# Kernel tuning notes

Hardware: AMD Instinct MI355X
Metric: run time of the kernel (lower is better)

The kernel has to match this reference:

```python
import jax, jax.numpy as jnp
import numpy as np

D = H = W = 64
N = D * H * W
BS = 2
C = 32          # enc_dim
IN_DIM = 4
OUT_DIM = 4
P = 5           # pos_enc_dim
COND = 32
M = 8           # modes per axis
NL = 4          # n_layers
NODE_IN = IN_DIM + 3 + 2 * P * 3   # 37
ENC_T = 1 + 2 * P                  # 11
ENC_C = ENC_T * COND               # 352
DT = 0.05


def fourier_embedding(pos, n_freq):
    # F(x) = [cos(2^i*pi*x_l), sin(2^i*pi*x_l)] per coordinate l, then concat x
    freq = (2.0 ** jnp.arange(n_freq, dtype=jnp.float32)) * jnp.pi  # (P,)
    ang = pos[..., None] * freq                                     # (..., L, P)
    emb = jnp.concatenate([jnp.cos(ang), jnp.sin(ang)], axis=-1)    # (..., L, 2P)
    emb = emb.reshape(*pos.shape[:-1], -1)                          # (..., L*2P)
    return jnp.concatenate([emb, pos], axis=-1)


def setup_inputs() -> dict:
    key = jax.random.key(0)
    ks = jax.random.split(key, 24)
    scale = 1.0 / C ** 2
    inp = {
        "state_in": jax.random.normal(ks[0], (BS, N, IN_DIM), jnp.float32),
        "node_pos": jax.random.uniform(ks[1], (BS, N, 3), jnp.float32),
        "edges": jax.random.randint(ks[2], (BS, 16, 2), 0, N),
        "time_i": jax.random.uniform(ks[3], (BS, 1), jnp.float32),
        "conditions": jax.random.uniform(ks[4], (BS, COND), jnp.float32),
        "t_embed_w": jax.random.normal(ks[5], (C, ENC_T), jnp.float32) * 0.05,
        "t_embed_b": jax.random.normal(ks[6], (C,), jnp.float32) * 0.05,
        "c_embed_w": jax.random.normal(ks[7], (C, ENC_C), jnp.float32) * 0.05,
        "c_embed_b": jax.random.normal(ks[8], (C,), jnp.float32) * 0.05,
        "lift_w": jax.random.normal(ks[9], (C, NODE_IN), jnp.float32) * 0.05,
        "lift_b": jax.random.normal(ks[10], (C,), jnp.float32) * 0.05,
        "spec_wr": jax.random.uniform(ks[11], (NL, C, C, M, M, M), jnp.float32) * scale,
        "spec_wi": jax.random.uniform(ks[12], (NL, C, C, M, M, M), jnp.float32) * scale,
        "byp_w": jax.random.normal(ks[13], (NL, C, C), jnp.float32) * 0.05,
        "byp_b": jax.random.normal(ks[14], (NL, C), jnp.float32) * 0.05,
        "proj1_w": jax.random.normal(ks[15], (C, C), jnp.float32) * 0.05,
        "proj1_b": jax.random.normal(ks[16], (C,), jnp.float32) * 0.05,
        "proj2_w": jax.random.normal(ks[17], (OUT_DIM, C), jnp.float32) * 0.05,
        "proj2_b": jax.random.normal(ks[18], (OUT_DIM,), jnp.float32) * 0.05,
    }
    return inp


def _conv1x1(x, w, b):
    # x: (b, c, d, h, w), w: (o, c), b: (o,)
    return jnp.einsum('bcdhw,oc->bodhw', x, w) + b[None, :, None, None, None]


def _fno_forward(state_in, node_pos, time_i, conditions,
                 t_embed_w, t_embed_b, c_embed_w, c_embed_b, lift_w, lift_b,
                 spec_wr, spec_wi, byp_w, byp_b, proj1_w, proj1_b, proj2_w, proj2_b):
    pos_enc = fourier_embedding(node_pos, P)      # (bs, N, 33)
    c_enc = fourier_embedding(conditions, P)      # (bs, 352)
    t_enc = fourier_embedding(time_i, P)          # (bs, 11)

    node_feat = jnp.concatenate([state_in, pos_enc], axis=-1)  # (bs, N, 37)
    t_emb = (t_enc @ t_embed_w.T + t_embed_b)[:, :, None, None, None]
    c_emb = (c_enc @ c_embed_w.T + c_embed_b)[:, :, None, None, None]

    # (bs, N, 37) -> (bs, 37, D, H, W)
    x = node_feat.transpose(0, 2, 1).reshape(BS, NODE_IN, D, H, W)
    x = _conv1x1(x, lift_w, lift_b)
    x = x + t_emb + c_emb

    for l in range(NL):
        w = jax.lax.complex(spec_wr[l], spec_wi[l])              # (C, C, M, M, M)
        x_ft = jnp.fft.rfftn(x, axes=(-3, -2, -1))               # (bs, C, D, H, W//2+1)
        blk = jnp.einsum('bixyz,ioxyz->boxyz', x_ft[..., :M, :M, :M], w)
        out_ft = jnp.zeros_like(x_ft).at[..., :M, :M, :M].set(blk)
        sp = jnp.fft.irfftn(out_ft, s=(D, H, W), axes=(-3, -2, -1))
        bp = _conv1x1(x, byp_w[l], byp_b[l])
        x = jax.nn.gelu(sp + bp, approximate=False)

    x = jax.nn.gelu(_conv1x1(x, proj1_w, proj1_b), approximate=False)
    x = _conv1x1(x, proj2_w, proj2_b)                            # (bs, 4, D, H, W)
    v_pred = x.reshape(BS, OUT_DIM, N).transpose(0, 2, 1)        # (bs, N, 4)
    return state_in + DT * v_pred


def reference(state_in, node_pos, edges, time_i, conditions,
              t_embed_w, t_embed_b, c_embed_w, c_embed_b, lift_w, lift_b,
              spec_wr, spec_wi, byp_w, byp_b, proj1_w, proj1_b, proj2_w, proj2_b):
    # edges are unused in the FNO forward (kept for API compatibility)
    return _fno_forward(state_in, node_pos, time_i, conditions,
                        t_embed_w, t_embed_b, c_embed_w, c_embed_b, lift_w, lift_b,
                        spec_wr, spec_wi, byp_w, byp_b, proj1_w, proj1_b, proj2_w, proj2_b)
```

## Files before the change

kernel.cpp:

```cpp
#include <hip/hip_runtime.h>
#include <math.h>

#define PI_F 3.14159265358979323846f

typedef __bf16 bf16x8 __attribute__((ext_vector_type(8)));
typedef float floatx4 __attribute__((ext_vector_type(4)));
union U8 { unsigned short u[8]; uint4 q; bf16x8 v; };

__device__ __forceinline__ float gelu_sig(float v) {
    float e = __builtin_amdgcn_exp2f(-2.4554670f * v);
    return v * __builtin_amdgcn_rcpf(1.0f + e);
}
__device__ __forceinline__ int rfl(int x) { return __builtin_amdgcn_readfirstlane(x); }

__device__ __forceinline__ unsigned short f2bf(float f) {
    unsigned int u = __float_as_uint(f);
    u += 0x7fffu + ((u >> 16) & 1u);
    return (unsigned short)(u >> 16);
}
__device__ __forceinline__ float bf2f(unsigned short h) {
    return __uint_as_float(((unsigned int)h) << 16);
}
__device__ __forceinline__ unsigned int pack2(float a, float b) {
    return (unsigned int)f2bf(a) | ((unsigned int)f2bf(b) << 16);
}

__global__ void k_wt(const float* __restrict__ time_i, const float* __restrict__ conditions,
                     const float* __restrict__ t_embed_w, const float* __restrict__ t_embed_b,
                     const float* __restrict__ c_embed_w, const float* __restrict__ c_embed_b,
                     const float* __restrict__ lift_b, float* __restrict__ embk,
                     const float* __restrict__ byp_w, const float* __restrict__ lift_w,
                     unsigned short* __restrict__ wbh, unsigned short* __restrict__ wlbf,
                     unsigned short* __restrict__ Tinv, unsigned short* __restrict__ TfT,
                     float* __restrict__ Tp1g) {
    const float th = PI_F / 32.0f;
    int t = threadIdx.x;
    if (blockIdx.x < 2) {
        __shared__ float red[8][32];
        int b = blockIdx.x;
        int c = t & 31, lg = t >> 5;
        float acc = 0.0f;
        if (lg == 0) {
            acc = t_embed_b[c] + c_embed_b[c] + lift_b[c];
            float tv = time_i[b];
            float ang = PI_F * tv;
            const float* tw = t_embed_w + c * 11;
            for (int i = 0; i < 5; i++) {
                float s, co; sincosf(ang, &s, &co);
                acc += co * tw[i] + s * tw[5 + i];
                ang *= 2.0f;
            }
            acc += tv * tw[10];
        }
        const float* cw = c_embed_w + c * 352;
        for (int j = 0; j < 4; j++) {
            int l = lg * 4 + j;
            float v = conditions[b * 32 + l];
            float ang = PI_F * v;
            for (int i = 0; i < 5; i++) {
                float s, co; sincosf(ang, &s, &co);
                acc += co * cw[l * 10 + i] + s * cw[l * 10 + 5 + i];
                ang *= 2.0f;
            }
            acc += v * cw[320 + l];
        }
        red[lg][c] = acc;
        __syncthreads();
        if (t < 32) {
            float s = 0.0f;
            for (int g = 0; g < 8; g++) s += red[g][t];
            embk[b * 32 + t] = s;
        }
        return;
    }
    int idx = (blockIdx.x - 2) * 256 + t;
    if (idx < 4096) {
        wbh[idx] = f2bf(byp_w[idx]);
    } else if (idx < 6144) {
        int j = idx - 4096;
        int o = j >> 6, q = j & 63;
        wlbf[j] = (q < 37) ? f2bf(lift_w[o * 37 + q]) : 0;
    } else if (idx < 8192) {
        int j = idx - 6144;
        int nz = j >> 5, k = j & 31;
        int kz = k >> 1;
        float val = 0.0f;
        if (kz < 8) {
            float a = (float)((kz * nz) & 63) * th;
            val = (k & 1) ? sinf(a) : cosf(a);
            val *= (kz == 0) ? (1.0f / 262144.0f) : (2.0f / 262144.0f);
        }
        Tinv[j] = f2bf(val);
    } else if (idx < 9216) {
        int j = idx - 8192;
        int kcol = j >> 6, nz = j & 63;
        int kz = kcol >> 1;
        float a = (float)((kz * nz) & 63) * th;
        float val = (kcol & 1) ? -sinf(a) : cosf(a);
        TfT[j] = f2bf(val);
    } else if (idx < 9728) {
        int j = idx - 9216;
        int ny = j >> 3, ky = j & 7;
        float a = (float)((ky * ny) & 63) * th;
        Tp1g[j * 2] = cosf(a);
        Tp1g[j * 2 + 1] = sinf(a);
    }
}

__device__ __forceinline__ void swz8k(int blk, int& b, int& nx, int& ny) {
    int x = blk & 7;
    int j = blk >> 3;
    int pair = x * 16 + (j >> 6);
    ny = j & 63;
    b = pair >> 6;
    nx = pair & 63;
}

__global__ __launch_bounds__(256) void k_lift(const float* __restrict__ state_in,
        const float* __restrict__ node_pos, const unsigned short* __restrict__ wlbf,
        const float* __restrict__ embk, const unsigned short* __restrict__ TfT,
        unsigned short* __restrict__ x0, unsigned int* __restrict__ a1) {
    __shared__ __align__(16) float SL[5024];
    unsigned short* fsT  = (unsigned short*)SL;
    unsigned short* ysbf = (unsigned short*)(SL + 2304);
    float* pz   = SL + 3456;
    float* pz2  = SL + 4480;
    float* bias = SL + 4992;
    int t = threadIdx.x;
    int b, nx, ny; swz8k(blockIdx.x, b, nx, ny);
    int nxy = nx * 64 + ny;

    if (t < 32) bias[t] = embk[b * 32 + t];
    {
        for (int u = t; u < 2048; u += 256) {
            int row = u >> 5, col = 37 + (u & 31);
            fsT[row * 72 + col] = 0;
        }
    }
    if (t < 192) {
        int nzf = t / 3;
        int l = t - nzf * 3;
        float p = node_pos[((size_t)b * 262144 + (nxy << 6)) * 3 + t];
        float s, c; sincosf(PI_F * p, &s, &c);
        unsigned short* row = fsT + nzf * 72;
        #pragma unroll
        for (int i = 0; i < 5; i++) {
            row[4 + l * 10 + i] = f2bf(c);
            row[4 + l * 10 + 5 + i] = f2bf(s);
            float nc = 2.0f * c * c - 1.0f;
            s = 2.0f * s * c;
            c = nc;
        }
        row[34 + l] = f2bf(p);
    } else {
        int nzf = t - 192;
        const float4 s4 = *(const float4*)(state_in + ((size_t)b * 262144 + (nxy << 6) + nzf) * 4);
        unsigned short* row = fsT + nzf * 72;
        row[0] = f2bf(s4.x); row[1] = f2bf(s4.y);
        row[2] = f2bf(s4.z); row[3] = f2bf(s4.w);
    }
    __syncthreads();

    int lane = t & 63;
    int w = rfl(t >> 6);
    int otile = w & 1;
    int nzt0 = (w >> 1) * 2;
    int l15 = lane & 15;
    int quad = lane >> 4;

    U8 a0, a1_;
    a0.q = *(const uint4*)(wlbf + ((otile * 16 + l15) << 6) + (quad << 3));
    a1_.q = *(const uint4*)(wlbf + ((otile * 16 + l15) << 6) + 32 + (quad << 3));
    floatx4 cb;
    #pragma unroll
    for (int r = 0; r < 4; r++) cb[r] = bias[otile * 16 + quad * 4 + r];
    floatx4 dz = {0.0f, 0.0f, 0.0f, 0.0f};

    #pragma unroll
    for (int m = 0; m < 2; m++) {
        int nzc = (nzt0 + m) * 16 + l15;
        U8 b0, b1_;
        b0.q = *(const uint4*)(fsT + nzc * 72 + (quad << 3));
        b1_.q = *(const uint4*)(fsT + nzc * 72 + 32 + (quad << 3));
        floatx4 d = __builtin_amdgcn_mfma_f32_16x16x32_bf16(a0.v, b0.v, cb, 0, 0, 0);
        d = __builtin_amdgcn_mfma_f32_16x16x32_bf16(a1_.v, b1_.v, d, 0, 0, 0);
        #pragma unroll
        for (int r = 0; r < 4; r++) {
            int o = otile * 16 + quad * 4 + r;
            ysbf[o * 72 + nzc] = f2bf(d[r]);
        }
    }
    __syncthreads();
    {
        int ch = t >> 3, q = t & 7;
        uint4 v = *(const uint4*)(ysbf + ch * 72 + q * 8);
        *(uint4*)(x0 + (((size_t)(b * 32 + ch)) << 18) + (nxy << 6) + q * 8) = v;
    }
    {
        int khalf = w >> 1;
        U8 ay, bt;
        ay.q = *(const uint4*)(ysbf + (otile * 16 + l15) * 72 + khalf * 32 + (quad << 3));
        bt.q = *(const uint4*)(TfT + (l15 << 6) + khalf * 32 + (quad << 3));
        floatx4 d = __builtin_amdgcn_mfma_f32_16x16x32_bf16(ay.v, bt.v, dz, 0, 0, 0);
        *(floatx4*)(pz + w * 256 + lane * 4) = d;
    }
    __syncthreads();
    if (w < 2) {
        float4 p0 = *(float4*)(pz + w * 256 + lane * 4);
        float4 p1 = *(float4*)(pz + (w + 2) * 256 + lane * 4);
        float pv[4] = {p0.x + p1.x, p0.y + p1.y, p0.z + p1.z, p0.w + p1.w};
        #pragma unroll
        for (int r = 0; r < 4; r++)
            pz2[(otile * 16 + quad * 4 + r) * 16 + l15] = pv[r];
    }
    __syncthreads();
    if (t < 128) {
        float4 v = *(float4*)(pz2 + t * 4);
        unsigned int* a1p = a1 + ((size_t)(b * 4096 + nxy)) * 256;
        *(uint2*)(a1p + t * 2) = make_uint2(pack2(v.x, v.y), pack2(v.z, v.w));
    }
}


__global__ __launch_bounds__(256) void k_p1(const unsigned int* __restrict__ a1,
        const float2* __restrict__ Tp1g, float2* __restrict__ a2p) {
    int blk = blockIdx.x, t = threadIdx.x;
    int x = blk & 7, r = blk >> 3;
    int pair = x * 16 + (r & 15);
    int qtr = r >> 4;
    const unsigned int* src = a1 + ((size_t)(pair * 64 + qtr * 16)) * 256 + t;
    float accr[8], acci[8];
    #pragma unroll
    for (int k = 0; k < 8; k++) { accr[k] = 0.0f; acci[k] = 0.0f; }
    #pragma unroll 4
    for (int j = 0; j < 16; j++) {
        int ny = qtr * 16 + j;
        unsigned int pv = src[(size_t)j * 256];
        float vx = bf2f((unsigned short)(pv & 0xffffu));
        float vy = bf2f((unsigned short)(pv >> 16));
        const float2* tw = Tp1g + ny * 8;
        #pragma unroll
        for (int ky = 0; ky < 8; ky++) {
            float2 w2 = tw[ky];
            accr[ky] += vx * w2.x + vy * w2.y;
            acci[ky] += vy * w2.x - vx * w2.y;
        }
    }
    float4* dst = (float4*)(a2p + (size_t)qtr * 262144 + ((size_t)(pair * 256 + t)) * 8);
    #pragma unroll
    for (int j = 0; j < 4; j++)
        dst[j] = make_float4(accr[2 * j], acci[2 * j], accr[2 * j + 1], acci[2 * j + 1]);
}

__global__ __launch_bounds__(256) void k_p2(const float2* __restrict__ a2p,
                                            float2* __restrict__ xft) {
    __shared__ __align__(16) float2 SH[1040];
    int blk = blockIdx.x, t = threadIdx.x;
    for (int lu = 0; lu < 2; lu++) {
        int un = blk * 2 + lu;
        int b = un >> 8, ckz = un & 255;
        size_t base = (size_t)b * 131072 + (size_t)ckz * 8;
        for (int e = t; e < 512; e += 256) {
            size_t a = base + (size_t)(e >> 3) * 2048 + (e & 7);
            float2 v0 = a2p[a];
            float2 v1 = a2p[a + 262144];
            float2 v2 = a2p[a + 524288];
            float2 v3 = a2p[a + 786432];
            SH[lu * 520 + e] = make_float2(v0.x + v1.x + v2.x + v3.x,
                                           v0.y + v1.y + v2.y + v3.y);
        }
    }
    __syncthreads();
    if (t < 128) {
        int lu = t >> 6, out = t & 63;
        int un = blk * 2 + lu;
        int kx = out & 7;
        float sn, cc; sincosf((float)kx * (PI_F / 32.0f), &sn, &cc);
        float bsn = -sn;
        float tc = 1.0f, ts = 0.0f, rr = 0.0f, ri = 0.0f;
        const float2* row = SH + lu * 520 + (out >> 3);
        for (int nx = 0; nx < 64; nx++) {
            float2 v = row[nx * 8];
            rr += v.x * tc - v.y * ts;
            ri += v.x * ts + v.y * tc;
            float nt = tc * cc - ts * bsn; ts = ts * cc + tc * bsn; tc = nt;
        }
        xft[(size_t)un * 64 + out] = make_float2(rr, ri);
    }
}

__global__ __launch_bounds__(256) void k_p3(const float2* __restrict__ xft,
        const float* __restrict__ wr, const float* __restrict__ wi,
        float2* __restrict__ yftp) {
    __shared__ __align__(16) float2 SH[64];
    int blk = blockIdx.x, t = threadIdx.x;
    int unit = blk >> 2, iq = blk & 3;
    int b = unit >> 6, kx = (unit >> 3) & 7, ky = unit & 7;
    if (t < 64) {
        int il = t >> 3, kz = t & 7;
        int i = iq * 8 + il;
        SH[t] = xft[((size_t)((b * 32 + i) * 8 + kz)) * 64 + ky * 8 + kx];
    }
    __syncthreads();
    int o = t >> 3, kz = t & 7;
    float yr = 0.0f, yi = 0.0f;
    for (int il = 0; il < 8; il++) {
        int i = iq * 8 + il;
        float2 xv = SH[il * 8 + kz];
        int wofs = ((i * 32 + o) << 9) + kx * 64 + ky * 8 + kz;
        float wrv = wr[wofs], wiv = wi[wofs];
        yr += xv.x * wrv - xv.y * wiv;
        yi += xv.x * wiv + xv.y * wrv;
    }
    yftp[(size_t)iq * 32768 + ((size_t)((b * 32 + o) * 8 + kz)) * 64 + ky * 8 + kx]
        = make_float2(yr, yi);
}

__global__ __launch_bounds__(256) void k_p4(const float2* __restrict__ yftp,
                                            float2* __restrict__ b1) {
    __shared__ __align__(16) float2 SH[4608];
    int blk = blockIdx.x, t = threadIdx.x;
    for (int u = 0; u < 2; u++) {
        if (u) __syncthreads();
        int unit = blk * 2 + u;
        int b = unit >> 8, nx = (unit >> 2) & 63, og = unit & 3;
        size_t sbase = ((size_t)(b * 32 + og * 8)) * 512;
        for (int e = t; e < 4096; e += 256) {
            float2 v0 = yftp[sbase + e];
            float2 v1 = yftp[32768 + sbase + e];
            float2 v2 = yftp[65536 + sbase + e];
            float2 v3 = yftp[98304 + sbase + e];
            SH[(e >> 3) * 9 + (e & 7)] = make_float2(v0.x + v1.x + v2.x + v3.x,
                                                     v0.y + v1.y + v2.y + v3.y);
        }
        __syncthreads();
        float cs, ss; sincosf((float)nx * (PI_F / 32.0f), &ss, &cs);
        float2* dst = b1 + ((size_t)(b * 64 + nx)) * 2048 + og * 512;
        for (int h = 0; h < 2; h++) {
            int idx = h * 256 + t;
            const float2* row = SH + idx * 9;
            float c = 1.0f, s = 0.0f, rr = 0.0f, ri = 0.0f;
            #pragma unroll
            for (int kx = 0; kx < 8; kx++) {
                float2 y = row[kx];
                rr += y.x * c - y.y * s;
                ri += y.x * s + y.y * c;
                float nc = c * cs - s * ss; s = s * cs + c * ss; c = nc;
            }
            dst[idx] = make_float2(rr, ri);
        }
    }
}

__global__ __launch_bounds__(256) void k_fin(
        const unsigned short* __restrict__ xin, const float2* __restrict__ b1,
        const unsigned short* __restrict__ wbh, const float* __restrict__ bb,
        const unsigned short* __restrict__ Tinv, const unsigned short* __restrict__ TfT,
        const float2* __restrict__ Tp1g, unsigned short* __restrict__ xout,
        unsigned int* __restrict__ a1, int do_z, int do_proj,
        const float* __restrict__ state_in, const float* __restrict__ p1w,
        const float* __restrict__ p1b, const float* __restrict__ p2w,
        const float* __restrict__ p2b, float* __restrict__ outp) {
    __shared__ __align__(16) float S[4416];
    float* pz   = S;
    float* pz2  = S + 1024;
    float* pr   = S;
    unsigned short* xsu  = (unsigned short*)(S + 1536);
    unsigned short* msbf = (unsigned short*)(S + 2592);
    unsigned short* ysbf = (unsigned short*)(S + 3232);
    float* bias = S + 4384;
    int t = threadIdx.x;
    int b, nx, ny; swz8k(blockIdx.x, b, nx, ny);
    int nxy = nx * 64 + ny;

    if (t >= 96 && t < 128) bias[t - 96] = bb[t - 96];
    ((unsigned int*)msbf)[(t >> 3) * 20 + 8 + (t & 7)] = 0;
    {
        int ch = t >> 3, q = t & 7;
        uint4 v = *(const uint4*)(xin + (((size_t)b) << 23) + (nxy << 6)
                                  + ((size_t)ch << 18) + q * 8);
        unsigned int* dst = (unsigned int*)(xsu + ch * 66 + q * 8);
        dst[0] = v.x; dst[1] = v.y; dst[2] = v.z; dst[3] = v.w;
    }
    {
        const float4* g = (const float4*)(b1 + ((size_t)(b * 64 + nx)) * 2048
                                          + (size_t)t * 8);
        float4 g0 = g[0], g1 = g[1], g2 = g[2], g3 = g[3];
        float vr[8], vi[8];
        vr[0] = g0.x; vi[0] = g0.y; vr[1] = g0.z; vi[1] = g0.w;
        vr[2] = g1.x; vi[2] = g1.y; vr[3] = g1.z; vi[3] = g1.w;
        vr[4] = g2.x; vi[4] = g2.y; vr[5] = g2.z; vi[5] = g2.w;
        vr[6] = g3.x; vi[6] = g3.y; vr[7] = g3.z; vi[7] = g3.w;
        const float2* tw = Tp1g + ny * 8;
        float mr = 0.0f, mi = 0.0f;
        #pragma unroll
        for (int ky = 0; ky < 8; ky++) {
            float2 w2 = tw[ky];
            mr += vr[ky] * w2.x - vi[ky] * w2.y;
            mi += vr[ky] * w2.y + vi[ky] * w2.x;
        }
        ((unsigned int*)msbf)[(t >> 3) * 20 + (t & 7)] = pack2(mr, -mi);
    }
    __syncthreads();

    int lane = t & 63;
    int w = rfl(t >> 6);
    int otile = w & 1;
    int nzt0 = (w >> 1) * 2;
    int l15 = lane & 15;
    int quad = lane >> 4;

    U8 aw, ams;
    aw.q = *(const uint4*)(wbh + ((otile * 16 + l15) << 5) + (quad << 3));
    ams.q = *(const uint4*)(msbf + (otile * 16 + l15) * 40 + (quad << 3));
    floatx4 cb;
    #pragma unroll
    for (int r = 0; r < 4; r++) cb[r] = bias[otile * 16 + quad * 4 + r];
    floatx4 dzero = {0.0f, 0.0f, 0.0f, 0.0f};

    size_t colbase = (((size_t)b) << 23) + (nxy << 6);

    #pragma unroll
    for (int m = 0; m < 2; m++) {
        int nzc = (nzt0 + m) * 16 + l15;
        U8 bx, bt;
        #pragma unroll
        for (int j = 0; j < 8; j++) bx.u[j] = xsu[(quad * 8 + j) * 66 + nzc];
        bt.q = *(const uint4*)(Tinv + (nzc << 5) + (quad << 3));
        floatx4 d = __builtin_amdgcn_mfma_f32_16x16x32_bf16(aw.v, bx.v, cb, 0, 0, 0);
        d = __builtin_amdgcn_mfma_f32_16x16x32_bf16(ams.v, bt.v, d, 0, 0, 0);
        #pragma unroll
        for (int r = 0; r < 4; r++) {
            int o = otile * 16 + quad * 4 + r;
            ysbf[o * 72 + nzc] = f2bf(gelu_sig(d[r]));
        }
    }
    __syncthreads();

    if (!do_proj) {
        int ch = t >> 3, q = t & 7;
        uint4 v = *(const uint4*)(ysbf + ch * 72 + q * 8);
        *(uint4*)(xout + colbase + ((size_t)ch << 18) + q * 8) = v;
    }

    if (do_z) {
        int khalf = w >> 1;
        U8 ay, bt;
        ay.q = *(const uint4*)(ysbf + (otile * 16 + l15) * 72 + khalf * 32 + (quad << 3));
        bt.q = *(const uint4*)(TfT + (l15 << 6) + khalf * 32 + (quad << 3));
        floatx4 d = __builtin_amdgcn_mfma_f32_16x16x32_bf16(ay.v, bt.v, dzero, 0, 0, 0);
        *(floatx4*)(pz + w * 256 + lane * 4) = d;
        __syncthreads();
        if (w < 2) {
            float4 p0 = *(float4*)(pz + w * 256 + lane * 4);
            float4 p1 = *(float4*)(pz + (w + 2) * 256 + lane * 4);
            float pv[4] = {p0.x + p1.x, p0.y + p1.y, p0.z + p1.z, p0.w + p1.w};
            #pragma unroll
            for (int r = 0; r < 4; r++)
                pz2[(otile * 16 + quad * 4 + r) * 16 + l15] = pv[r];
        }
        __syncthreads();
        if (t < 128) {
            float4 v = *(float4*)(pz2 + t * 4);
            unsigned int* a1p = a1 + ((size_t)(b * 4096 + nxy)) * 256;
            *(uint2*)(a1p + t * 2) = make_uint2(pack2(v.x, v.y), pack2(v.z, v.w));
        }
    }

    if (do_proj) {
        int nz = t & 63;
        float xv[32];
        #pragma unroll
        for (int i = 0; i < 32; i++) xv[i] = bf2f(ysbf[i * 72 + nz]);
        float r0 = 0.f, r1 = 0.f, r2 = 0.f, r3 = 0.f;
        #pragma unroll
        for (int k = 0; k < 8; k++) {
            int o = w * 8 + k;
            float a = p1b[o];
            const float* wr = p1w + o * 32;
            #pragma unroll
            for (int i = 0; i < 32; i++) a += wr[i] * xv[i];
            float h = gelu_sig(a);
            r0 += p2w[0 * 32 + o] * h;
            r1 += p2w[1 * 32 + o] * h;
            r2 += p2w[2 * 32 + o] * h;
            r3 += p2w[3 * 32 + o] * h;
        }
        *(float4*)(pr + w * 256 + nz * 4) = make_float4(r0, r1, r2, r3);
        __syncthreads();
        if (t < 64) {
            float4 a0 = *(float4*)(pr + 0 * 256 + t * 4);
            float4 a1_ = *(float4*)(pr + 1 * 256 + t * 4);
            float4 a2 = *(float4*)(pr + 2 * 256 + t * 4);
            float4 a3 = *(float4*)(pr + 3 * 256 + t * 4);
            size_t base = ((size_t)b * 262144 + (nxy << 6) + t) * 4;
            float4 sv = *(const float4*)(state_in + base);
            *(float4*)(outp + base) = make_float4(
                sv.x + 0.05f * (p2b[0] + a0.x + a1_.x + a2.x + a3.x),
                sv.y + 0.05f * (p2b[1] + a0.y + a1_.y + a2.y + a3.y),
                sv.z + 0.05f * (p2b[2] + a0.z + a1_.z + a2.z + a3.z),
                sv.w + 0.05f * (p2b[3] + a0.w + a1_.w + a2.w + a3.w));
        }
    }
}

extern "C" void kernel_launch(void* const* d_in, const int* in_sizes, int n_in,
                              void* d_out, int out_size, void* d_ws, size_t ws_size,
                              hipStream_t stream) {
    const float* state_in   = (const float*)d_in[0];
    const float* node_pos   = (const float*)d_in[1];
    const float* time_i     = (const float*)d_in[3];
    const float* conditions = (const float*)d_in[4];
    const float* t_embed_w  = (const float*)d_in[5];
    const float* t_embed_b  = (const float*)d_in[6];
    const float* c_embed_w  = (const float*)d_in[7];
    const float* c_embed_b  = (const float*)d_in[8];
    const float* lift_w     = (const float*)d_in[9];
    const float* lift_b     = (const float*)d_in[10];
    const float* spec_wr    = (const float*)d_in[11];
    const float* spec_wi    = (const float*)d_in[12];
    const float* byp_w      = (const float*)d_in[13];
    const float* byp_b      = (const float*)d_in[14];
    const float* proj1_w    = (const float*)d_in[15];
    const float* proj1_b    = (const float*)d_in[16];
    const float* proj2_w    = (const float*)d_in[17];
    const float* proj2_b    = (const float*)d_in[18];
    float* out = (float*)d_out;
    float* ws  = (float*)d_ws;

    unsigned short* xA = (unsigned short*)ws;
    unsigned short* xB = (unsigned short*)(ws + 8388608);
    unsigned int* a1 = (unsigned int*)(ws + 16777216);
    float2* a2p  = (float2*)(ws + 20971520);
    float2* xft  = (float2*)(ws + 23068672);
    float2* yftp = (float2*)(ws + 23134208);
    float2* b1   = (float2*)(ws + 23396352);
    float*  embk = ws + 23920640;
    unsigned short* wbh  = (unsigned short*)(ws + 23920704);
    unsigned short* wlbf = (unsigned short*)(ws + 23922752);
    unsigned short* Tinv = (unsigned short*)(ws + 23923776);
    unsigned short* TfT  = (unsigned short*)(ws + 23924800);
    float* Tp1gf = ws + 23925312;
    float2* Tp1g = (float2*)Tp1gf;

    k_wt<<<40, 256, 0, stream>>>(time_i, conditions, t_embed_w, t_embed_b,
                                 c_embed_w, c_embed_b, lift_b, embk,
                                 byp_w, lift_w, wbh, wlbf, Tinv, TfT, Tp1gf);
    k_lift<<<8192, 256, 0, stream>>>(state_in, node_pos, wlbf, embk, TfT, xA, a1);

    for (int l = 0; l < 4; l++) {
        unsigned short* xin  = (l & 1) ? xB : xA;
        unsigned short* xout = (l & 1) ? xA : xB;
        const float* wrl = spec_wr + (size_t)l * 524288;
        const float* wil = spec_wi + (size_t)l * 524288;
        k_p1<<<512, 256, 0, stream>>>(a1, Tp1g, a2p);
        k_p2<<<256, 256, 0, stream>>>(a2p, xft);
        k_p3<<<512, 256, 0, stream>>>(xft, wrl, wil, yftp);
        k_p4<<<256, 256, 0, stream>>>(yftp, b1);
        k_fin<<<8192, 256, 0, stream>>>(xin, b1, wbh + l * 1024, byp_b + l * 32,
                                        Tinv, TfT, Tp1g, xout, a1, (l < 3) ? 1 : 0,
                                        (l == 3) ? 1 : 0, state_in,
                                        proj1_w, proj1_b, proj2_w, proj2_b, out);
    }
}
```

Before: 341.1 us.

## Store activations channel-last per column and fuse z-DFT into two waves

```diff
diff --git a/kernel.cpp b/kernel.cpp
--- a/kernel.cpp
+++ b/kernel.cpp
@@ -23,6 +23,11 @@
 }
 __device__ __forceinline__ unsigned int pack2(float a, float b) {
     return (unsigned int)f2bf(a) | ((unsigned int)f2bf(b) << 16);
+}
+__device__ __forceinline__ uint2 pack4h(unsigned short a, unsigned short b,
+                                        unsigned short c, unsigned short d) {
+    return make_uint2((unsigned int)a | ((unsigned int)b << 16),
+                      (unsigned int)c | ((unsigned int)d << 16));
 }
 
 __global__ void k_wt(const float* __restrict__ time_i, const float* __restrict__ conditions,
@@ -120,12 +125,10 @@
         const float* __restrict__ node_pos, const unsigned short* __restrict__ wlbf,
         const float* __restrict__ embk, const unsigned short* __restrict__ TfT,
         unsigned short* __restrict__ x0, unsigned int* __restrict__ a1) {
-    __shared__ __align__(16) float SL[5024];
+    __shared__ __align__(16) float SL[3488];
     unsigned short* fsT  = (unsigned short*)SL;
     unsigned short* ysbf = (unsigned short*)(SL + 2304);
-    float* pz   = SL + 3456;
-    float* pz2  = SL + 4480;
-    float* bias = SL + 4992;
+    float* bias = SL + 3456;
     int t = threadIdx.x;
     int b, nx, ny; swz8k(blockIdx.x, b, nx, ny);
     int nxy = nx * 64 + ny;
@@ -163,61 +166,55 @@
 
     int lane = t & 63;
     int w = rfl(t >> 6);
-    int otile = w & 1;
-    int nzt0 = (w >> 1) * 2;
     int l15 = lane & 15;
     int quad = lane >> 4;
-
-    U8 a0, a1_;
-    a0.q = *(const uint4*)(wlbf + ((otile * 16 + l15) << 6) + (quad << 3));
-    a1_.q = *(const uint4*)(wlbf + ((otile * 16 + l15) << 6) + 32 + (quad << 3));
-    floatx4 cb;
+    int nz = w * 16 + l15;
+    size_t xbase = ((size_t)(b * 4096 + nxy)) * 2048;
+
+    U8 b0, b1_;
+    b0.q  = *(const uint4*)(fsT + nz * 72 + (quad << 3));
+    b1_.q = *(const uint4*)(fsT + nz * 72 + 32 + (quad << 3));
     #pragma unroll
-    for (int r = 0; r < 4; r++) cb[r] = bias[otile * 16 + quad * 4 + r];
-    floatx4 dz = {0.0f, 0.0f, 0.0f, 0.0f};
-
-    #pragma unroll
-    for (int m = 0; m < 2; m++) {
-        int nzc = (nzt0 + m) * 16 + l15;
-        U8 b0, b1_;
-        b0.q = *(const uint4*)(fsT + nzc * 72 + (quad << 3));
-        b1_.q = *(const uint4*)(fsT + nzc * 72 + 32 + (quad << 3));
-        floatx4 d = __builtin_amdgcn_mfma_f32_16x16x32_bf16(a0.v, b0.v, cb, 0, 0, 0);
-        d = __builtin_amdgcn_mfma_f32_16x16x32_bf16(a1_.v, b1_.v, d, 0, 0, 0);
+    for (int ot = 0; ot < 2; ot++) {
+        U8 aA, aB;
+        aA.q = *(const uint4*)(wlbf + ((ot * 16 + l15) << 6) + (quad << 3));
+        aB.q = *(const uint4*)(wlbf + ((ot * 16 + l15) << 6) + 32 + (quad << 3));
+        floatx4 cb;
+        #pragma unroll
+        for (int r = 0; r < 4; r++) cb[r] = bias[ot * 16 + quad * 4 + r];
+        floatx4 d = __builtin_amdgcn_mfma_f32_16x16x32_bf16(aA.v, b0.v, cb, 0, 0, 0);
+        d = __builtin_amdgcn_mfma_f32_16x16x32_bf16(aB.v, b1_.v, d, 0, 0, 0);
+        unsigned short h[4];
         #pragma unroll
         for (int r = 0; r < 4; r++) {
-            int o = otile * 16 + quad * 4 + r;
-            ysbf[o * 72 + nzc] = f2bf(d[r]);
-        }
+            h[r] = f2bf(d[r]);
+            ysbf[(ot * 16 + quad * 4 + r) * 72 + nz] = h[r];
+        }
+        *(uint2*)(x0 + xbase + nz * 32 + ot * 16 + (quad << 2)) =
+            pack4h(h[0], h[1], h[2], h[3]);
     }
     __syncthreads();
-    {
-        int ch = t >> 3, q = t & 7;
-        uint4 v = *(const uint4*)(ysbf + ch * 72 + q * 8);
-        *(uint4*)(x0 + (((size_t)(b * 32 + ch)) << 18) + (nxy << 6) + q * 8) = v;
-    }
-    {
-        int khalf = w >> 1;
-        U8 ay, bt;
-        ay.q = *(const uint4*)(ysbf + (otile * 16 + l15) * 72 + khalf * 32 + (quad << 3));
-        bt.q = *(const uint4*)(TfT + (l15 << 6) + khalf * 32 + (quad << 3));
-        floatx4 d = __builtin_amdgcn_mfma_f32_16x16x32_bf16(ay.v, bt.v, dz, 0, 0, 0);
-        *(floatx4*)(pz + w * 256 + lane * 4) = d;
-    }
-    __syncthreads();
+
     if (w < 2) {
-        float4 p0 = *(float4*)(pz + w * 256 + lane * 4);
-        float4 p1 = *(float4*)(pz + (w + 2) * 256 + lane * 4);
-        float pv[4] = {p0.x + p1.x, p0.y + p1.y, p0.z + p1.z, p0.w + p1.w};
-        #pragma unroll
-        for (int r = 0; r < 4; r++)
-            pz2[(otile * 16 + quad * 4 + r) * 16 + l15] = pv[r];
-    }
-    __syncthreads();
-    if (t < 128) {
-        float4 v = *(float4*)(pz2 + t * 4);
-        unsigned int* a1p = a1 + ((size_t)(b * 4096 + nxy)) * 256;
-        *(uint2*)(a1p + t * 2) = make_uint2(pack2(v.x, v.y), pack2(v.z, v.w));
+        int o = w * 16 + l15;
+        U8 ay0, ay1, bt0, bt1;
+        ay0.q = *(const uint4*)(ysbf + o * 72 + (quad << 3));
+        ay1.q = *(const uint4*)(ysbf + o * 72 + 32 + (quad << 3));
+        bt0.q = *(const uint4*)(TfT + (l15 << 6) + (quad << 3));
+        bt1.q = *(const uint4*)(TfT + (l15 << 6) + 32 + (quad << 3));
+        floatx4 z = {0.0f, 0.0f, 0.0f, 0.0f};
+        z = __builtin_amdgcn_mfma_f32_16x16x32_bf16(ay0.v, bt0.v, z, 0, 0, 0);
+        z = __builtin_amdgcn_mfma_f32_16x16x32_bf16(ay1.v, bt1.v, z, 0, 0, 0);
+        float p0 = __shfl_xor(z[0], 1), p1 = __shfl_xor(z[1], 1);
+        float p2 = __shfl_xor(z[2], 1), p3 = __shfl_xor(z[3], 1);
+        if (!(lane & 1)) {
+            unsigned int* a1p = a1 + ((size_t)(b * 4096 + nxy)) * 256;
+            int kz = l15 >> 1;
+            a1p[(w * 16 + quad * 4 + 0) * 8 + kz] = pack2(z[0], p0);
+            a1p[(w * 16 + quad * 4 + 1) * 8 + kz] = pack2(z[1], p1);
+            a1p[(w * 16 + quad * 4 + 2) * 8 + kz] = pack2(z[2], p2);
+            a1p[(w * 16 + quad * 4 + 3) * 8 + kz] = pack2(z[3], p3);
+        }
     }
 }
 
@@ -361,27 +358,29 @@
         const float* __restrict__ state_in, const float* __restrict__ p1w,
         const float* __restrict__ p1b, const float* __restrict__ p2w,
         const float* __restrict__ p2b, float* __restrict__ outp) {
-    __shared__ __align__(16) float S[4416];
-    float* pz   = S;
-    float* pz2  = S + 1024;
-    float* pr   = S;
-    unsigned short* xsu  = (unsigned short*)(S + 1536);
-    unsigned short* msbf = (unsigned short*)(S + 2592);
-    unsigned short* ysbf = (unsigned short*)(S + 3232);
-    float* bias = S + 4384;
+    __shared__ __align__(16) float S[2848];
+    float* pr = S;
+    unsigned short* msbf = (unsigned short*)(S + 1024);
+    unsigned short* ysbf = (unsigned short*)(S + 1664);
+    float* bias = S + 2816;
     int t = threadIdx.x;
     int b, nx, ny; swz8k(blockIdx.x, b, nx, ny);
     int nxy = nx * 64 + ny;
+    int lane = t & 63;
+    int w = rfl(t >> 6);
+    int l15 = lane & 15;
+    int quad = lane >> 4;
+    int nz = w * 16 + l15;
+    size_t xbase = ((size_t)(b * 4096 + nxy)) * 2048;
+
+    U8 bx, btv, aw0, aw1;
+    bx.q  = *(const uint4*)(xin + xbase + nz * 32 + (quad << 3));
+    btv.q = *(const uint4*)(Tinv + (nz << 5) + (quad << 3));
+    aw0.q = *(const uint4*)(wbh + (l15 << 5) + (quad << 3));
+    aw1.q = *(const uint4*)(wbh + ((16 + l15) << 5) + (quad << 3));
 
     if (t >= 96 && t < 128) bias[t - 96] = bb[t - 96];
     ((unsigned int*)msbf)[(t >> 3) * 20 + 8 + (t & 7)] = 0;
-    {
-        int ch = t >> 3, q = t & 7;
-        uint4 v = *(const uint4*)(xin + (((size_t)b) << 23) + (nxy << 6)
-                                  + ((size_t)ch << 18) + q * 8);
-        unsigned int* dst = (unsigned int*)(xsu + ch * 66 + q * 8);
-        dst[0] = v.x; dst[1] = v.y; dst[2] = v.z; dst[3] = v.w;
-    }
     {
         const float4* g = (const float4*)(b1 + ((size_t)(b * 64 + nx)) * 2048
                                           + (size_t)t * 8);
@@ -403,75 +402,63 @@
     }
     __syncthreads();
 
-    int lane = t & 63;
-    int w = rfl(t >> 6);
-    int otile = w & 1;
-    int nzt0 = (w >> 1) * 2;
-    int l15 = lane & 15;
-    int quad = lane >> 4;
-
-    U8 aw, ams;
-    aw.q = *(const uint4*)(wbh + ((otile * 16 + l15) << 5) + (quad << 3));
-    ams.q = *(const uint4*)(msbf + (otile * 16 + l15) * 40 + (quad << 3));
-    floatx4 cb;
+    U8 am0, am1;
+    am0.q = *(const uint4*)(msbf + l15 * 40 + (quad << 3));
+    am1.q = *(const uint4*)(msbf + (16 + l15) * 40 + (quad << 3));
+    floatx4 cb0, cb1;
     #pragma unroll
-    for (int r = 0; r < 4; r++) cb[r] = bias[otile * 16 + quad * 4 + r];
-    floatx4 dzero = {0.0f, 0.0f, 0.0f, 0.0f};
-
-    size_t colbase = (((size_t)b) << 23) + (nxy << 6);
-
+    for (int r = 0; r < 4; r++) {
+        cb0[r] = bias[quad * 4 + r];
+        cb1[r] = bias[16 + quad * 4 + r];
+    }
+    floatx4 d0 = __builtin_amdgcn_mfma_f32_16x16x32_bf16(aw0.v, bx.v, cb0, 0, 0, 0);
+    d0 = __builtin_amdgcn_mfma_f32_16x16x32_bf16(am0.v, btv.v, d0, 0, 0, 0);
+    floatx4 d1 = __builtin_amdgcn_mfma_f32_16x16x32_bf16(aw1.v, bx.v, cb1, 0, 0, 0);
+    d1 = __builtin_amdgcn_mfma_f32_16x16x32_bf16(am1.v, btv.v, d1, 0, 0, 0);
+
+    unsigned short h0[4], h1[4];
     #pragma unroll
-    for (int m = 0; m < 2; m++) {
-        int nzc = (nzt0 + m) * 16 + l15;
-        U8 bx, bt;
-        #pragma unroll
-        for (int j = 0; j < 8; j++) bx.u[j] = xsu[(quad * 8 + j) * 66 + nzc];
-        bt.q = *(const uint4*)(Tinv + (nzc << 5) + (quad << 3));
-        floatx4 d = __builtin_amdgcn_mfma_f32_16x16x32_bf16(aw.v, bx.v, cb, 0, 0, 0);
-        d = __builtin_amdgcn_mfma_f32_16x16x32_bf16(ams.v, bt.v, d, 0, 0, 0);
-        #pragma unroll
-        for (int r = 0; r < 4; r++) {
-            int o = otile * 16 + quad * 4 + r;
-            ysbf[o * 72 + nzc] = f2bf(gelu_sig(d[r]));
-        }
+    for (int r = 0; r < 4; r++) {
+        h0[r] = f2bf(gelu_sig(d0[r]));
+        ysbf[(quad * 4 + r) * 72 + nz] = h0[r];
+        h1[r] = f2bf(gelu_sig(d1[r]));
+        ysbf[(16 + quad * 4 + r) * 72 + nz] = h1[r];
+    }
+    if (!do_proj) {
+        *(uint2*)(xout + xbase + nz * 32 + (quad << 2)) =
+            pack4h(h0[0], h0[1], h0[2], h0[3]);
+        *(uint2*)(xout + xbase + nz * 32 + 16 + (quad << 2)) =
+            pack4h(h1[0], h1[1], h1[2], h1[3]);
     }
     __syncthreads();
 
-    if (!do_proj) {
-        int ch = t >> 3, q = t & 7;
-        uint4 v = *(const uint4*)(ysbf + ch * 72 + q * 8);
-        *(uint4*)(xout + colbase + ((size_t)ch << 18) + q * 8) = v;
-    }
-
-    if (do_z) {
-        int khalf = w >> 1;
-        U8 ay, bt;
-        ay.q = *(const uint4*)(ysbf + (otile * 16 + l15) * 72 + khalf * 32 + (quad << 3));
-        bt.q = *(const uint4*)(TfT + (l15 << 6) + khalf * 32 + (quad << 3));
-        floatx4 d = __builtin_amdgcn_mfma_f32_16x16x32_bf16(ay.v, bt.v, dzero, 0, 0, 0);
-        *(floatx4*)(pz + w * 256 + lane * 4) = d;
-        __syncthreads();
-        if (w < 2) {
-            float4 p0 = *(float4*)(pz + w * 256 + lane * 4);
-            float4 p1 = *(float4*)(pz + (w + 2) * 256 + lane * 4);
-            float pv[4] = {p0.x + p1.x, p0.y + p1.y, p0.z + p1.z, p0.w + p1.w};
-            #pragma unroll
-            for (int r = 0; r < 4; r++)
-                pz2[(otile * 16 + quad * 4 + r) * 16 + l15] = pv[r];
-        }
-        __syncthreads();
-        if (t < 128) {
-            float4 v = *(float4*)(pz2 + t * 4);
+    if (do_z && w < 2) {
+        int o = w * 16 + l15;
+        U8 ay0, ay1, bt0, bt1;
+        ay0.q = *(const uint4*)(ysbf + o * 72 + (quad << 3));
+        ay1.q = *(const uint4*)(ysbf + o * 72 + 32 + (quad << 3));
+        bt0.q = *(const uint4*)(TfT + (l15 << 6) + (quad << 3));
+        bt1.q = *(const uint4*)(TfT + (l15 << 6) + 32 + (quad << 3));
+        floatx4 z = {0.0f, 0.0f, 0.0f, 0.0f};
+        z = __builtin_amdgcn_mfma_f32_16x16x32_bf16(ay0.v, bt0.v, z, 0, 0, 0);
+        z = __builtin_amdgcn_mfma_f32_16x16x32_bf16(ay1.v, bt1.v, z, 0, 0, 0);
+        float p0 = __shfl_xor(z[0], 1), p1 = __shfl_xor(z[1], 1);
+        float p2 = __shfl_xor(z[2], 1), p3 = __shfl_xor(z[3], 1);
+        if (!(lane & 1)) {
             unsigned int* a1p = a1 + ((size_t)(b * 4096 + nxy)) * 256;
-            *(uint2*)(a1p + t * 2) = make_uint2(pack2(v.x, v.y), pack2(v.z, v.w));
+            int kz = l15 >> 1;
+            a1p[(w * 16 + quad * 4 + 0) * 8 + kz] = pack2(z[0], p0);
+            a1p[(w * 16 + quad * 4 + 1) * 8 + kz] = pack2(z[1], p1);
+            a1p[(w * 16 + quad * 4 + 2) * 8 + kz] = pack2(z[2], p2);
+            a1p[(w * 16 + quad * 4 + 3) * 8 + kz] = pack2(z[3], p3);
         }
     }
 
     if (do_proj) {
-        int nz = t & 63;
+        int nzp = t & 63;
         float xv[32];
         #pragma unroll
-        for (int i = 0; i < 32; i++) xv[i] = bf2f(ysbf[i * 72 + nz]);
+        for (int i = 0; i < 32; i++) xv[i] = bf2f(ysbf[i * 72 + nzp]);
         float r0 = 0.f, r1 = 0.f, r2 = 0.f, r3 = 0.f;
         #pragma unroll
         for (int k = 0; k < 8; k++) {
@@ -486,7 +473,7 @@
             r2 += p2w[2 * 32 + o] * h;
             r3 += p2w[3 * 32 + o] * h;
         }
-        *(float4*)(pr + w * 256 + nz * 4) = make_float4(r0, r1, r2, r3);
+        *(float4*)(pr + w * 256 + nzp * 4) = make_float4(r0, r1, r2, r3);
         __syncthreads();
         if (t < 64) {
             float4 a0 = *(float4*)(pr + 0 * 256 + t * 4);
```

Result: slower. 351.7 us (+3.1%).
